# Performance work log

Measured on AMD Instinct MI355X. Metric: run time of the kernel, lower is better.

Reference implementation:

```python
import jax, jax.numpy as jnp
import numpy as np

NUM_CLASS = 80
S = 76              # output_size = 608 // 8 (scale i=0)
STRIDE = 8.0
XYSCALE = 1.2
IOU_LOSS_THRESH = 0.5
INPUT_SIZE = 608.0  # stride * output_size
ANCHORS0 = np.array([[12., 16.], [19., 36.], [40., 28.]], dtype=np.float32)


def setup_inputs() -> dict:
    key = jax.random.key(0)
    k1, k2, k3 = jax.random.split(key, 3)
    B, MAXGT = 16, 150
    conv = jax.random.normal(k1, (B, S, S, 3 * (5 + NUM_CLASS)), dtype=jnp.float32)
    label = jax.random.uniform(k2, (B, S, S, 3, 5 + NUM_CLASS), dtype=jnp.float32)
    # scale the xywh channels of label to pixel coordinates
    label = label.at[..., :4].multiply(INPUT_SIZE)
    bboxes = jax.random.uniform(k3, (B, MAXGT, 4), dtype=jnp.float32) * INPUT_SIZE
    return {"conv": conv, "label": label, "bboxes": bboxes}


def _bce_with_logits(logits, labels):
    # tf.nn.sigmoid_cross_entropy_with_logits, numerically stable form
    return jnp.maximum(logits, 0.0) - logits * labels + jnp.log1p(jnp.exp(-jnp.abs(logits)))


def _xywh_to_corners(b):
    return jnp.concatenate([b[..., :2] - b[..., 2:] * 0.5,
                            b[..., :2] + b[..., 2:] * 0.5], axis=-1)


def _bbox_iou(boxes1, boxes2):
    area1 = boxes1[..., 2] * boxes1[..., 3]
    area2 = boxes2[..., 2] * boxes2[..., 3]
    b1, b2 = _xywh_to_corners(boxes1), _xywh_to_corners(boxes2)
    lu = jnp.maximum(b1[..., :2], b2[..., :2])
    rd = jnp.minimum(b1[..., 2:], b2[..., 2:])
    inter = jnp.maximum(rd - lu, 0.0)
    inter_area = inter[..., 0] * inter[..., 1]
    union = area1 + area2 - inter_area
    return inter_area / union


def _bbox_giou(boxes1, boxes2):
    area1 = boxes1[..., 2] * boxes1[..., 3]
    area2 = boxes2[..., 2] * boxes2[..., 3]
    b1, b2 = _xywh_to_corners(boxes1), _xywh_to_corners(boxes2)
    lu = jnp.maximum(b1[..., :2], b2[..., :2])
    rd = jnp.minimum(b1[..., 2:], b2[..., 2:])
    inter = jnp.maximum(rd - lu, 0.0)
    inter_area = inter[..., 0] * inter[..., 1]
    union = area1 + area2 - inter_area
    iou = inter_area / union
    enc_lu = jnp.minimum(b1[..., :2], b2[..., :2])
    enc_rd = jnp.maximum(b1[..., 2:], b2[..., 2:])
    enc = jnp.maximum(enc_rd - enc_lu, 0.0)
    enc_area = enc[..., 0] * enc[..., 1]
    return iou - (enc_area - union) / enc_area


def _decode_train(conv):
    B = conv.shape[0]
    conv = conv.reshape(B, S, S, 3, 5 + NUM_CLASS)
    dxdy, dwdh, raw_conf, raw_prob = jnp.split(conv, [2, 4, 5], axis=-1)
    xs, ys = jnp.meshgrid(jnp.arange(S), jnp.arange(S))  # indexing='xy' like tf.meshgrid
    grid = jnp.stack([xs, ys], axis=-1)[None, :, :, None, :].astype(jnp.float32)  # [1,S,S,1,2]
    pred_xy = (jax.nn.sigmoid(dxdy) * XYSCALE - 0.5 * (XYSCALE - 1.0) + grid) * STRIDE
    pred_wh = jnp.exp(dwdh) * ANCHORS0  # [B,S,S,3,2]
    return jnp.concatenate([pred_xy, pred_wh,
                            jax.nn.sigmoid(raw_conf), jax.nn.sigmoid(raw_prob)], axis=-1)


def reference(conv, label, bboxes):
    pred = _decode_train(conv)  # [B,S,S,3,5+C]
    B = conv.shape[0]
    conv5 = conv.reshape(B, S, S, 3, 5 + NUM_CLASS)
    conv_raw_conf = conv5[..., 4:5]
    conv_raw_prob = conv5[..., 5:]

    pred_xywh = pred[..., 0:4]
    pred_conf = pred[..., 4:5]

    label_xywh = label[..., 0:4]
    respond_bbox = label[..., 4:5]
    label_prob = label[..., 5:]

    giou = _bbox_giou(pred_xywh, label_xywh)[..., None]
    bbox_loss_scale = 2.0 - label_xywh[..., 2:3] * label_xywh[..., 3:4] / (INPUT_SIZE ** 2)
    giou_loss = respond_bbox * bbox_loss_scale * (1.0 - giou)

    # pairwise IoU: [B,S,S,3,1,4] vs [B,1,1,1,MAXGT,4] -> [B,S,S,3,MAXGT]
    iou = _bbox_iou(pred_xywh[..., None, :], bboxes[:, None, None, None, :, :])
    max_iou = jnp.max(iou, axis=-1, keepdims=True)
    respond_bgd = (1.0 - respond_bbox) * (max_iou < IOU_LOSS_THRESH).astype(jnp.float32)

    conf_focal = jnp.square(respond_bbox - pred_conf)
    bce_conf = _bce_with_logits(conv_raw_conf, respond_bbox)
    conf_loss = conf_focal * (respond_bbox * bce_conf + respond_bgd * bce_conf)
    prob_loss = respond_bbox * _bce_with_logits(conv_raw_prob, label_prob)

    giou_loss = jnp.mean(jnp.sum(giou_loss, axis=(1, 2, 3, 4)))
    conf_loss = jnp.mean(jnp.sum(conf_loss, axis=(1, 2, 3, 4)))
    prob_loss = jnp.mean(jnp.sum(prob_loss, axis=(1, 2, 3, 4)))
    return jnp.stack([giou_loss, conf_loss, prob_loss])
```

## Files before the change

kernel.cpp:

```cpp
#include <hip/hip_runtime.h>
#include <math.h>

#define S 76
#define A 3
#define CH 85
#define MAXGT 150
#define CPB (S * S * A)
#define FPB (CPB * CH)
#define BATCH 16
#define TOTF4 ((BATCH * FPB) / 4)
#define BLK 256
#define ROUNDS 8
#define DEPTH 4
#define STREAM_BLOCKS ((TOTF4 + BLK * ROUNDS - 1) / (BLK * ROUNDS))
#define ATILE 128
#define AGX ((CPB + ATILE - 1) / ATILE)
#define GEO_BLOCKS (AGX * BATCH)
#define TOT_BLOCKS (STREAM_BLOCKS + GEO_BLOCKS)
#define MAXC 392

typedef float fx4 __attribute__((ext_vector_type(4)));

__device__ __forceinline__ float frcp(float x) { return __builtin_amdgcn_rcpf(x); }
__device__ __forceinline__ float sigmoidf_(float x) { return frcp(1.f + __expf(-x)); }
__device__ __forceinline__ float bcef(float x, float y) {
    const float t  = __builtin_amdgcn_exp2f(x * 1.44269504f);
    const float lg = __builtin_amdgcn_logf(1.f + t);
    return __builtin_fmaf(0.69314718f, lg, -x * y);
}

template<int N>
__device__ __forceinline__ void vmwait() {
    asm volatile("s_waitcnt vmcnt(%0)" :: "i"(N));
    __builtin_amdgcn_sched_barrier(0);
}
__device__ __forceinline__ void gload4(fx4& d, const float* p) {
    asm volatile("global_load_dwordx4 %0, %1, off" : "=v"(d) : "v"(p));
}

__global__ __launch_bounds__(BLK, 6) void yolo_fused_kernel(
    const float* __restrict__ conv, const float* __restrict__ label,
    const float* __restrict__ bboxes, float* __restrict__ partA ,
    float* __restrict__ partB )
{
    __shared__ float  s_resp[MAXC];
    __shared__ float  sredp[BLK / 64];
    __shared__ float4 s_box[MAXGT];
    __shared__ float  s_ba[MAXGT];
    __shared__ float  sred2[2][BLK / 64];

    const unsigned bid = blockIdx.x;
    const int tid = threadIdx.x;
    const unsigned geo_before = (unsigned)(((unsigned long long)bid * GEO_BLOCKS) / TOT_BLOCKS);
    const unsigned geo_after  = (unsigned)(((unsigned long long)(bid + 1) * GEO_BLOCKS) / TOT_BLOCKS);

    if (geo_after == geo_before) {
        const unsigned sidx = bid - geo_before;
        const int base = (int)sidx * (BLK * ROUNDS);
        float p_sum = 0.f;

        if (sidx + 1 < STREAM_BLOCKS) {
            const unsigned base_e = 4u * (unsigned)base;
            const unsigned cstart = base_e / 85u;
            const unsigned cend   = (base_e + BLK * ROUNDS * 4u - 1u) / 85u;
            const int nc = (int)(cend - cstart) + 1;
            for (int i = tid; i < nc; i += BLK)
                s_resp[i] = label[(size_t)(cstart + i) * CH + 4];
            __syncthreads();

            const float* pc0 = conv  + ((size_t)base + (size_t)tid) * 4;
            const float* pl0 = label + ((size_t)base + (size_t)tid) * 4;
            fx4 c_s[DEPTH], l_s[DEPTH];
            #pragma unroll
            for (int s = 0; s < DEPTH; ++s) {
                gload4(c_s[s], pc0 + s * (BLK * 4));
                gload4(l_s[s], pl0 + s * (BLK * 4));
            }
            #define STEP(R, W)                                                      \
            {                                                                       \
                vmwait<W>();                                                        \
                const fx4 cc = c_s[(R) & 3];                                        \
                const fx4 lc = l_s[(R) & 3];                                        \
                const unsigned e0 = 4u * (unsigned)(base + (R) * BLK + tid);        \
                const unsigned c0 = e0 / 85u;                                       \
                const unsigned r0 = e0 - 85u * c0;                                  \
                const float rsp = s_resp[c0 - cstart];                              \
                const float cxx[4] = {cc.x, cc.y, cc.z, cc.w};                      \
                const float lxx[4] = {lc.x, lc.y, lc.z, lc.w};                      \
                float s_ = 0.f;                                                     \
                _Pragma("unroll")                                                   \
                for (int k = 0; k < 4; ++k) {                                       \
                    const unsigned rr = r0 + (unsigned)k;                           \
                    const float bv = bcef(cxx[k], lxx[k]);                          \
                    s_ += ((rr - 5u) < 80u) ? bv : 0.f;                             \
                }                                                                   \
                p_sum = __builtin_fmaf(rsp, s_, p_sum);                             \
                if ((R) + DEPTH < ROUNDS) {                                         \
                    gload4(c_s[(R) & 3], pc0 + ((R) + DEPTH) * (BLK * 4));          \
                    gload4(l_s[(R) & 3], pl0 + ((R) + DEPTH) * (BLK * 4));          \
                }                                                                   \
            }
            STEP(0, 6) STEP(1, 6) STEP(2, 6) STEP(3, 6)
            STEP(4, 6) STEP(5, 4) STEP(6, 2) STEP(7, 0)
            #undef STEP
        } else {
            const float4* cv4 = (const float4*)conv;
            const float4* lb4 = (const float4*)label;
            for (int r = 0; r < ROUNDS; ++r) {
                const int u = base + r * BLK + tid;
                if (u >= TOTF4) break;
                const float4 cc = cv4[(size_t)u];
                const float4 lc = lb4[(size_t)u];
                const unsigned e0 = 4u * (unsigned)u;
                const unsigned c0 = e0 / 85u;
                const unsigned r0c = e0 - 85u * c0;
                const float rspc = label[(size_t)c0 * CH + 4];
                const float cxx[4] = {cc.x, cc.y, cc.z, cc.w};
                const float lxx[4] = {lc.x, lc.y, lc.z, lc.w};
                float s_ = 0.f;
                #pragma unroll
                for (int k = 0; k < 4; ++k) {
                    const unsigned rr = r0c + k;
                    const float bv = bcef(cxx[k], lxx[k]);
                    s_ += ((rr - 5u) < 80u) ? bv : 0.f;
                }
                p_sum = __builtin_fmaf(rspc, s_, p_sum);
            }
        }

        for (int off = 32; off > 0; off >>= 1) p_sum += __shfl_down(p_sum, off, 64);
        const int lane = tid & 63, wv = tid >> 6;
        if (lane == 0) sredp[wv] = p_sum;
        __syncthreads();
        if (tid == 0) {
            float P = 0.f;
            #pragma unroll
            for (int w = 0; w < BLK / 64; ++w) P += sredp[w];
            partB[sidx] = P;
        }
    } else {
        const unsigned gidx = geo_before;
        const int b    = gidx / AGX;
        const int tile = gidx - b * AGX;

        const int ci = tid >> 1;
        const int pr = tid & 1;
        const int t = tile * ATILE + ci;
        const bool valid = (t < CPB);
        const int tc = valid ? t : (CPB - 1);

        const size_t boff = (size_t)b * FPB;
        const float* cv = conv  + boff + (size_t)tc * CH;
        const float* lb = label + boff + (size_t)tc * CH;

        if (tid < MAXGT) {
            const float4 bx = *(const float4*)(bboxes + (size_t)b * (MAXGT * 4) + tid * 4);
            const float hw = bx.z * 0.5f, hh = bx.w * 0.5f;
            s_box[tid] = make_float4(3.f * (bx.x - hw), bx.y - hh, 3.f * (bx.x + hw), bx.y + hh);
            s_ba[tid]  = bx.z * bx.w;
        }
        const float dx = cv[0], dy = cv[1], dw = cv[2], dh = cv[3], rc = cv[4];
        const float lx = lb[0], ly = lb[1], lw = lb[2], lh = lb[3], resp = lb[4];
        __syncthreads();

        const int i   = tc / (S * A);
        const int rem = tc - i * (S * A);
        const int j   = rem / A;
        const int a   = rem - j * A;
        const float aw = (a == 0) ? 12.f : ((a == 1) ? 19.f : 40.f);
        const float ah = (a == 0) ? 16.f : ((a == 1) ? 36.f : 28.f);

        const float px = (sigmoidf_(dx) * 1.2f - 0.1f + (float)j) * 8.f;
        const float py = (sigmoidf_(dy) * 1.2f - 0.1f + (float)i) * 8.f;
        const float pw = __expf(dw) * aw;
        const float ph = __expf(dh) * ah;
        const float pconf = sigmoidf_(rc);

        const float px1 = px - pw * 0.5f, py1 = py - ph * 0.5f;
        const float px2 = px + pw * 0.5f, py2 = py + ph * 0.5f;
        const float areap = pw * ph;

        const float px1_3 = 3.f * px1, px2_3 = 3.f * px2;
        float maxv = -1e30f;
        #pragma unroll 5
        for (int k = pr; k < MAXGT; k += 2) {
            const float4 bx = s_box[k];
            const float ba  = s_ba[k];
            const float kiw3 = fmaxf(fminf(px2_3, bx.z) - fmaxf(px1_3, bx.x), 0.f);
            const float kih  = fmaxf(fminf(py2, bx.w) - fmaxf(py1, bx.y), 0.f);
            maxv = fmaxf(maxv, __builtin_fmaf(kiw3, kih, -ba));
        }
        maxv = fmaxf(maxv, __shfl_xor(maxv, 1, 64));

        float g_sum = 0.f, c_sum = 0.f;
        if (pr == 0 && valid) {
            const float lx1 = lx - lw * 0.5f, ly1 = ly - lh * 0.5f;
            const float lx2 = lx + lw * 0.5f, ly2 = ly + lh * 0.5f;
            const float areal = lw * lh;
            const float iw = fmaxf(fminf(px2, lx2) - fmaxf(px1, lx1), 0.f);
            const float ih = fmaxf(fminf(py2, ly2) - fmaxf(py1, ly1), 0.f);
            const float inter = iw * ih;
            const float uni = areap + areal - inter;
            const float iou = inter * frcp(uni);
            const float ew = fmaxf(fmaxf(px2, lx2) - fminf(px1, lx1), 0.f);
            const float eh = fmaxf(fmaxf(py2, ly2) - fminf(py1, ly1), 0.f);
            const float enc = ew * eh;
            const float giou = iou - (enc - uni) * frcp(enc);
            g_sum = resp * (2.f - areal * (1.f / (608.f * 608.f))) * (1.f - giou);

            const float bgd = (1.f - resp) * ((maxv < areap) ? 1.f : 0.f);
            const float focal = (resp - pconf) * (resp - pconf);
            c_sum = focal * (resp + bgd) * bcef(rc, resp);
        }

        for (int off = 32; off > 0; off >>= 1) {
            g_sum += __shfl_down(g_sum, off, 64);
            c_sum += __shfl_down(c_sum, off, 64);
        }
        const int lane = tid & 63, wv = tid >> 6;
        if (lane == 0) { sred2[0][wv] = g_sum; sred2[1][wv] = c_sum; }
        __syncthreads();
        if (tid == 0) {
            float G = 0.f, C = 0.f;
            #pragma unroll
            for (int w = 0; w < BLK / 64; ++w) { G += sred2[0][w]; C += sred2[1][w]; }
            partA[gidx * 2 + 0] = G;
            partA[gidx * 2 + 1] = C;
        }
    }
}

__global__ __launch_bounds__(256) void final_reduce(
    const float* __restrict__ partA, const float* __restrict__ partB,
    float* __restrict__ out, int nA, int nB, float invB)
{
    const int tid = threadIdx.x;
    float g = 0.f, c = 0.f, p = 0.f;
    for (int k = tid; k < nA; k += 256) { g += partA[2 * k]; c += partA[2 * k + 1]; }
    for (int k = tid; k < nB; k += 256) p += partB[k];
    for (int off = 32; off > 0; off >>= 1) {
        g += __shfl_down(g, off, 64);
        c += __shfl_down(c, off, 64);
        p += __shfl_down(p, off, 64);
    }
    __shared__ float sred[3][4];
    const int lane = tid & 63, wv = tid >> 6;
    if (lane == 0) { sred[0][wv] = g; sred[1][wv] = c; sred[2][wv] = p; }
    __syncthreads();
    if (tid == 0) {
        float G = 0.f, C = 0.f, P = 0.f;
        #pragma unroll
        for (int w = 0; w < 4; ++w) { G += sred[0][w]; C += sred[1][w]; P += sred[2][w]; }
        out[0] = G * invB;
        out[1] = C * invB;
        out[2] = P * invB;
    }
}

extern "C" void kernel_launch(void* const* d_in, const int* in_sizes, int n_in,
                              void* d_out, int out_size, void* d_ws, size_t ws_size,
                              hipStream_t stream) {
    const float* conv   = (const float*)d_in[0];
    const float* label  = (const float*)d_in[1];
    const float* bboxes = (const float*)d_in[2];
    float* out  = (float*)d_out;
    float* wsf  = (float*)d_ws;
    float* partA = wsf;
    float* partB = wsf + 8192;

    yolo_fused_kernel<<<TOT_BLOCKS, BLK, 0, stream>>>(conv, label, bboxes, partA, partB);
    final_reduce<<<1, 256, 0, stream>>>(partA, partB, out, GEO_BLOCKS, STREAM_BLOCKS,
                                        1.f / (float)BATCH);
}
```

Baseline: 64.03 us.

## Stream conv/label via global-to-LDS async loads with per-wave contiguous chunks

The streaming BCE path now uses global_load_lds (16-byte) to copy conv and label tiles straight into LDS through a 3-deep per-wave ring buffer, instead of register-destination dwordx4 loads. Each wave walks its own contiguous chunk, and each block covers twice as many rounds, so there are fewer stream blocks. Shared memory is unified into one char buffer aliased differently for the stream and geometry branches, and the occupancy hint in launch_bounds is dropped. The aim is to cut VGPR pressure and keep more bytes in flight, at the cost of an extra LDS round-trip per element and more LDS per block.

```diff
diff --git a/kernel.cpp b/kernel.cpp
--- a/kernel.cpp
+++ b/kernel.cpp
@@ -10,14 +10,16 @@
 #define BATCH 16
 #define TOTF4 ((BATCH * FPB) / 4)
 #define BLK 256
-#define ROUNDS 8
-#define DEPTH 4
-#define STREAM_BLOCKS ((TOTF4 + BLK * ROUNDS - 1) / (BLK * ROUNDS))
+#define WPB (BLK / 64)
+#define ROUNDS 16
+#define DEPTH 3
+#define SPAN (BLK * ROUNDS)
+#define STREAM_BLOCKS ((TOTF4 + SPAN - 1) / SPAN)
 #define ATILE 128
 #define AGX ((CPB + ATILE - 1) / ATILE)
 #define GEO_BLOCKS (AGX * BATCH)
 #define TOT_BLOCKS (STREAM_BLOCKS + GEO_BLOCKS)
-#define MAXC 392
+#define MAXC 200
 
 typedef float fx4 __attribute__((ext_vector_type(4)));
 
@@ -31,57 +33,66 @@
 
 template<int N>
 __device__ __forceinline__ void vmwait() {
-    asm volatile("s_waitcnt vmcnt(%0)" :: "i"(N));
+    asm volatile("s_waitcnt vmcnt(%0)" :: "i"(N) : "memory");
     __builtin_amdgcn_sched_barrier(0);
 }
-__device__ __forceinline__ void gload4(fx4& d, const float* p) {
-    asm volatile("global_load_dwordx4 %0, %1, off" : "=v"(d) : "v"(p));
-}
-
-__global__ __launch_bounds__(BLK, 6) void yolo_fused_kernel(
+__device__ __forceinline__ void gl_lds16(const float* g, void* l) {
+    __builtin_amdgcn_global_load_lds(
+        (const __attribute__((address_space(1))) void*)g,
+        (__attribute__((address_space(3))) void*)l, 16, 0, 0);
+}
+
+__global__ __launch_bounds__(BLK) void yolo_fused_kernel(
     const float* __restrict__ conv, const float* __restrict__ label,
     const float* __restrict__ bboxes, float* __restrict__ partA ,
     float* __restrict__ partB )
 {
-    __shared__ float  s_resp[MAXC];
-    __shared__ float  sredp[BLK / 64];
-    __shared__ float4 s_box[MAXGT];
-    __shared__ float  s_ba[MAXGT];
-    __shared__ float  sred2[2][BLK / 64];
+    __shared__ __align__(16) char smem[25392];
 
     const unsigned bid = blockIdx.x;
-    const int tid = threadIdx.x;
+    const int tid  = threadIdx.x;
+    const int w    = tid >> 6;
+    const int lane = tid & 63;
     const unsigned geo_before = (unsigned)(((unsigned long long)bid * GEO_BLOCKS) / TOT_BLOCKS);
     const unsigned geo_after  = (unsigned)(((unsigned long long)(bid + 1) * GEO_BLOCKS) / TOT_BLOCKS);
 
     if (geo_after == geo_before) {
+        fx4*   lds_c  = (fx4*)smem;
+        fx4*   lds_l  = (fx4*)(smem + 12288);
+        float* s_resp = (float*)(smem + 24576);
+        float* sredp  = (float*)(smem + 25376);
+
         const unsigned sidx = bid - geo_before;
-        const int base = (int)sidx * (BLK * ROUNDS);
+        const int base4 = (int)sidx * SPAN;
         float p_sum = 0.f;
 
         if (sidx + 1 < STREAM_BLOCKS) {
-            const unsigned base_e = 4u * (unsigned)base;
+            const unsigned base_e = 4u * (unsigned)base4;
             const unsigned cstart = base_e / 85u;
-            const unsigned cend   = (base_e + BLK * ROUNDS * 4u - 1u) / 85u;
+            const unsigned cend   = (base_e + SPAN * 4u - 1u) / 85u;
             const int nc = (int)(cend - cstart) + 1;
-            for (int i = tid; i < nc; i += BLK)
-                s_resp[i] = label[(size_t)(cstart + i) * CH + 4];
+            for (int i2 = tid; i2 < nc; i2 += BLK)
+                s_resp[i2] = label[(size_t)(cstart + i2) * CH + 4];
             __syncthreads();
 
-            const float* pc0 = conv  + ((size_t)base + (size_t)tid) * 4;
-            const float* pl0 = label + ((size_t)base + (size_t)tid) * 4;
-            fx4 c_s[DEPTH], l_s[DEPTH];
-            #pragma unroll
-            for (int s = 0; s < DEPTH; ++s) {
-                gload4(c_s[s], pc0 + s * (BLK * 4));
-                gload4(l_s[s], pl0 + s * (BLK * 4));
-            }
-            #define STEP(R, W)                                                      \
+            const float* pc = conv  + ((size_t)base4 + (size_t)w * (ROUNDS * 64) + (size_t)lane) * 4;
+            const float* pl = label + ((size_t)base4 + (size_t)w * (ROUNDS * 64) + (size_t)lane) * 4;
+
+            #define ISSUE(R)                                                        \
+                gl_lds16(pc + (size_t)(R) * 256, &lds_c[(w * DEPTH + (R) % DEPTH) * 64]); \
+                gl_lds16(pl + (size_t)(R) * 256, &lds_l[(w * DEPTH + (R) % DEPTH) * 64]);
+
+            ISSUE(0) ISSUE(1) ISSUE(2)
+
+            #define STEPX(R, W)                                                     \
             {                                                                       \
                 vmwait<W>();                                                        \
-                const fx4 cc = c_s[(R) & 3];                                        \
-                const fx4 lc = l_s[(R) & 3];                                        \
-                const unsigned e0 = 4u * (unsigned)(base + (R) * BLK + tid);        \
+                fx4 cc = lds_c[(w * DEPTH + (R) % DEPTH) * 64 + lane];              \
+                fx4 lc = lds_l[(w * DEPTH + (R) % DEPTH) * 64 + lane];              \
+                asm volatile("s_waitcnt lgkmcnt(0)" ::: "memory");                  \
+                __builtin_amdgcn_sched_barrier(0);                                  \
+                if ((R) + DEPTH < ROUNDS) { ISSUE((R) + DEPTH) }                    \
+                const unsigned e0 = 4u * (unsigned)(base4 + w * (ROUNDS * 64) + (R) * 64 + lane); \
                 const unsigned c0 = e0 / 85u;                                       \
                 const unsigned r0 = e0 - 85u * c0;                                  \
                 const float rsp = s_resp[c0 - cstart];                              \
@@ -95,19 +106,18 @@
                     s_ += ((rr - 5u) < 80u) ? bv : 0.f;                             \
                 }                                                                   \
                 p_sum = __builtin_fmaf(rsp, s_, p_sum);                             \
-                if ((R) + DEPTH < ROUNDS) {                                         \
-                    gload4(c_s[(R) & 3], pc0 + ((R) + DEPTH) * (BLK * 4));          \
-                    gload4(l_s[(R) & 3], pl0 + ((R) + DEPTH) * (BLK * 4));          \
-                }                                                                   \
             }
-            STEP(0, 6) STEP(1, 6) STEP(2, 6) STEP(3, 6)
-            STEP(4, 6) STEP(5, 4) STEP(6, 2) STEP(7, 0)
-            #undef STEP
+            STEPX(0, 4)  STEPX(1, 4)  STEPX(2, 4)  STEPX(3, 4)
+            STEPX(4, 4)  STEPX(5, 4)  STEPX(6, 4)  STEPX(7, 4)
+            STEPX(8, 4)  STEPX(9, 4)  STEPX(10, 4) STEPX(11, 4)
+            STEPX(12, 4) STEPX(13, 4) STEPX(14, 2) STEPX(15, 0)
+            #undef STEPX
+            #undef ISSUE
         } else {
             const float4* cv4 = (const float4*)conv;
             const float4* lb4 = (const float4*)label;
             for (int r = 0; r < ROUNDS; ++r) {
-                const int u = base + r * BLK + tid;
+                const int u = base4 + r * BLK + tid;
                 if (u >= TOTF4) break;
                 const float4 cc = cv4[(size_t)u];
                 const float4 lc = lb4[(size_t)u];
@@ -129,16 +139,19 @@
         }
 
         for (int off = 32; off > 0; off >>= 1) p_sum += __shfl_down(p_sum, off, 64);
-        const int lane = tid & 63, wv = tid >> 6;
-        if (lane == 0) sredp[wv] = p_sum;
+        if (lane == 0) sredp[w] = p_sum;
         __syncthreads();
         if (tid == 0) {
             float P = 0.f;
             #pragma unroll
-            for (int w = 0; w < BLK / 64; ++w) P += sredp[w];
+            for (int q = 0; q < WPB; ++q) P += sredp[q];
             partB[sidx] = P;
         }
     } else {
+        fx4*   s_box  = (fx4*)smem;
+        float* s_ba   = (float*)(smem + 2400);
+        float* sred2  = (float*)(smem + 3000);
+
         const unsigned gidx = geo_before;
         const int b    = gidx / AGX;
         const int tile = gidx - b * AGX;
@@ -156,7 +169,9 @@
         if (tid < MAXGT) {
             const float4 bx = *(const float4*)(bboxes + (size_t)b * (MAXGT * 4) + tid * 4);
             const float hw = bx.z * 0.5f, hh = bx.w * 0.5f;
-            s_box[tid] = make_float4(3.f * (bx.x - hw), bx.y - hh, 3.f * (bx.x + hw), bx.y + hh);
+            fx4 v; v.x = 3.f * (bx.x - hw); v.y = bx.y - hh;
+            v.z = 3.f * (bx.x + hw); v.w = bx.y + hh;
+            s_box[tid] = v;
             s_ba[tid]  = bx.z * bx.w;
         }
         const float dx = cv[0], dy = cv[1], dw = cv[2], dh = cv[3], rc = cv[4];
@@ -184,7 +199,7 @@
         float maxv = -1e30f;
         #pragma unroll 5
         for (int k = pr; k < MAXGT; k += 2) {
-            const float4 bx = s_box[k];
+            const fx4 bx = s_box[k];
             const float ba  = s_ba[k];
             const float kiw3 = fmaxf(fminf(px2_3, bx.z) - fmaxf(px1_3, bx.x), 0.f);
             const float kih  = fmaxf(fminf(py2, bx.w) - fmaxf(py1, bx.y), 0.f);
@@ -217,13 +232,12 @@
             g_sum += __shfl_down(g_sum, off, 64);
             c_sum += __shfl_down(c_sum, off, 64);
         }
-        const int lane = tid & 63, wv = tid >> 6;
-        if (lane == 0) { sred2[0][wv] = g_sum; sred2[1][wv] = c_sum; }
+        if (lane == 0) { sred2[0 * WPB + w] = g_sum; sred2[1 * WPB + w] = c_sum; }
         __syncthreads();
         if (tid == 0) {
             float G = 0.f, C = 0.f;
             #pragma unroll
-            for (int w = 0; w < BLK / 64; ++w) { G += sred2[0][w]; C += sred2[1][w]; }
+            for (int q = 0; q < WPB; ++q) { G += sred2[q]; C += sred2[WPB + q]; }
             partA[gidx * 2 + 0] = G;
             partA[gidx * 2 + 1] = C;
         }
@@ -250,7 +264,7 @@
     if (tid == 0) {
         float G = 0.f, C = 0.f, P = 0.f;
         #pragma unroll
-        for (int w = 0; w < 4; ++w) { G += sred[0][w]; C += sred[1][w]; P += sred[2][w]; }
+        for (int q = 0; q < 4; ++q) { G += sred[0][q]; C += sred[1][q]; P += sred[2][q]; }
         out[0] = G * invB;
         out[1] = C * invB;
         out[2] = P * invB;
```

New measurement: 54.86 us. 14.3% less time.
